# Optimization experiments

Measured on AMD Instinct MI355X. Metric: run time of the kernel, lower is better.

## Reference

```python
import jax, jax.numpy as jnp
import numpy as np

LN_EPS = 1e-5  # torch nn.LayerNorm default
ATT_EPS = 1e-8  # episilon added to sqrt(dk)

B, S, D = 16, 2048, 1024


def setup_inputs() -> dict:
    key = jax.random.key(0)
    ks = jax.random.split(key, 5)
    Q = jax.random.normal(ks[0], (B, S, D), dtype=jnp.float32)
    K = jax.random.normal(ks[1], (B, S, D), dtype=jnp.float32)
    V = jax.random.normal(ks[2], (B, S, D), dtype=jnp.float32)
    # xavier_normal for square DxD: std = sqrt(2/(D+D)) = 1/sqrt(D)
    std = 1.0 / np.sqrt(D)
    W1 = jax.random.normal(ks[3], (D, D), dtype=jnp.float32) * std
    W2 = jax.random.normal(ks[4], (D, D), dtype=jnp.float32) * std
    b1 = jnp.zeros((D,), dtype=jnp.float32)
    b2 = jnp.zeros((D,), dtype=jnp.float32)
    ln_gamma = jnp.ones((D,), dtype=jnp.float32)
    ln_beta = jnp.zeros((D,), dtype=jnp.float32)
    return {"Q": Q, "K": K, "V": V, "W1": W1, "b1": b1, "W2": W2, "b2": b2,
            "ln_gamma": ln_gamma, "ln_beta": ln_beta}


def _layer_norm(x, gamma, beta):
    mu = jnp.mean(x, axis=-1, keepdims=True)
    var = jnp.mean(jnp.square(x - mu), axis=-1, keepdims=True)
    return (x - mu) * jax.lax.rsqrt(var + LN_EPS) * gamma + beta


def reference(Q, K, V, W1, b1, W2, b2, ln_gamma, ln_beta):
    d = Q.shape[-1]
    scale = 1.0 / (jnp.sqrt(jnp.float32(max(1.0, d))) + ATT_EPS)
    # scores: (B, Sq, Sk)
    scores = jnp.einsum('bqd,bkd->bqk', Q, K) * scale
    attn = jax.nn.softmax(scores, axis=-1)
    V_att = jnp.einsum('bqk,bkd->bqd', attn, V)
    X = _layer_norm(Q + V_att, ln_gamma, ln_beta)
    ffn = jnp.einsum('bqd,ed->bqe', jax.nn.relu(jnp.einsum('bqd,hd->bqh', X, W1) + b1), W2) + b2
    return _layer_norm(ffn + X, ln_gamma, ln_beta)
```

## Files before the change

kernel.cpp:

```cpp
#include <hip/hip_runtime.h>
#include <cmath>
#include <cstdint>

#define LN_EPS 1e-5f

typedef __bf16 bf16x8 __attribute__((ext_vector_type(8)));
typedef float f32x4 __attribute__((ext_vector_type(4)));
typedef unsigned short u16x8 __attribute__((ext_vector_type(8)));
typedef unsigned short u16x4 __attribute__((ext_vector_type(4)));

__device__ inline float b2f(unsigned short u) {
    union { unsigned int ui; float f; } x; x.ui = ((unsigned int)u) << 16; return x.f;
}
__device__ inline unsigned short f2b(float f) {
    union { float f; unsigned int ui; } x; x.f = f;
    unsigned int u = x.ui;
    return (unsigned short)((u + 0x7FFFu + ((u >> 16) & 1u)) >> 16);
}

__global__ void cvt2_kernel(const float* __restrict__ ia, unsigned short* __restrict__ oa,
                            long na, float sa,
                            const float* __restrict__ ib, unsigned short* __restrict__ ob,
                            long nb) {
    long i = ((long)blockIdx.x * blockDim.x + threadIdx.x) * 8;
    long stride = (long)gridDim.x * blockDim.x * 8;
    long n = na + nb;
    for (; i < n; i += stride) {
        const float* in; unsigned short* out; long j; float s;
        if (i < na) { in = ia; out = oa; j = i; s = sa; }
        else        { in = ib; out = ob; j = i - na; s = 1.0f; }
        float4 a = *reinterpret_cast<const float4*>(in + j);
        float4 b = *reinterpret_cast<const float4*>(in + j + 4);
        u16x8 o;
        o[0] = f2b(a.x * s); o[1] = f2b(a.y * s); o[2] = f2b(a.z * s); o[3] = f2b(a.w * s);
        o[4] = f2b(b.x * s); o[5] = f2b(b.y * s); o[6] = f2b(b.z * s); o[7] = f2b(b.w * s);
        *reinterpret_cast<u16x8*>(out + j) = o;
    }
}

__global__ void transpose_kernel(const float* __restrict__ V, unsigned short* __restrict__ Vt,
                                 int S, int D) {
    __shared__ float t[32][33];
    int b = blockIdx.z;
    int s0 = blockIdx.x * 32, d0 = blockIdx.y * 32;
    int tx = threadIdx.x & 31, ty = threadIdx.x >> 5;
    const float* Vb = V + (long)b * S * D;
    unsigned short* Vtb = Vt + (long)b * S * D;
#pragma unroll
    for (int r = 0; r < 4; ++r)
        t[ty + r * 8][tx] = Vb[(long)(s0 + ty + r * 8) * D + d0 + tx];
    __syncthreads();
#pragma unroll
    for (int r = 0; r < 4; ++r)
        Vtb[(long)(d0 + ty + r * 8) * S + s0 + tx] = f2b(t[tx][ty + r * 8]);
}

#define GBK 64

__device__ inline void gload16(const unsigned short* g, unsigned short* l) {
    __builtin_amdgcn_global_load_lds((const __attribute__((address_space(1))) void*)g,
                                     (__attribute__((address_space(3))) void*)l, 16, 0, 0);
}

__device__ inline void stage_half(const unsigned short* gRowBase, int ldk, int k0,
                                  unsigned short* ldsHalf, int tid) {
#pragma unroll
    for (int l = 0; l < 2; ++l) {
        int g = l * 512 + tid;
        int row = g >> 3;
        int lg = (g & 7) ^ (row & 7);
        gload16(gRowBase + (long)row * ldk + k0 + lg * 8, ldsHalf + g * 8);
    }
}

__device__ inline bf16x8 frag_ld(const unsigned short* ldsHalf, int rowInHalf, int kgran) {
    int sw = kgran ^ (rowInHalf & 7);
    return *reinterpret_cast<const bf16x8*>(ldsHalf + rowInHalf * 64 + sw * 8);
}

#define GMFMA(am, bn, mi, ni) \
    acc[mi][ni] = __builtin_amdgcn_mfma_f32_16x16x32_bf16(am, bn, acc[mi][ni], 0, 0, 0)

template <int MODE>
__global__ __launch_bounds__(512, 1) void gemm256(
    const unsigned short* __restrict__ A, const unsigned short* __restrict__ B,
    void* __restrict__ Cout, const float* __restrict__ aux1, const float* __restrict__ aux2,
    float* __restrict__ aux3, float* __restrict__ aux4,
    int tX, int tY, int N, int K, long bsA, long bsB, long bsC, float scale) {
    extern __shared__ __align__(16) unsigned short lds[];
    const int cpx = gridDim.x >> 3;
    const int swz = (blockIdx.x & 7) * cpx + (blockIdx.x >> 3);
    const int bx = swz % tX;
    const int t2 = swz / tX;
    const int by = t2 % tY, bz = t2 / tY;

    const unsigned short* Ab = A + (long)bz * bsA + (long)by * 256 * K;
    const unsigned short* Bb = B + (long)bz * bsB + (long)bx * 256 * K;
    const int tid = threadIdx.x;
    const int wid = tid >> 6, lane = tid & 63;
    const int wr = wid >> 2, wc = wid & 3;
    const int lr = lane & 15, kq = lane >> 4;
    const int NT = K >> 6;
    const int ccol = lane & 15, crow0 = kq * 4;
    const long m0 = (long)by * 256 + wr * 128;
    const long n0 = (long)bx * 256 + wc * 64;
    const int bRow0 = (wc & 1) * 64;

#define STAGE_A(tile, half) stage_half(Ab + (long)(half) * 128 * K, K, (tile) * GBK, \
        lds + (((tile) & 1) * 32768 + (half) * 8192), tid)
#define STAGE_B(tile, half) stage_half(Bb + (long)(half) * 128 * K, K, (tile) * GBK, \
        lds + (((tile) & 1) * 32768 + 16384 + (half) * 8192), tid)

    f32x4 acc[8][4];
#pragma unroll
    for (int i = 0; i < 8; ++i)
#pragma unroll
        for (int j = 0; j < 4; ++j) acc[i][j] = (f32x4){0.f, 0.f, 0.f, 0.f};
    bf16x8 a[4][2], b[4][2];

    STAGE_A(0, 0); STAGE_A(0, 1); STAGE_B(0, 0); STAGE_B(0, 1);
    STAGE_B(1, 0); STAGE_A(1, 0);
    asm volatile("s_waitcnt vmcnt(4)" ::: "memory");
    __builtin_amdgcn_s_barrier();

    for (int t = 0; t < NT; ++t) {
        const unsigned short* aB = lds + ((t & 1) * 32768 + wr * 8192);
        const unsigned short* bB = lds + ((t & 1) * 32768 + 16384 + (wc >> 1) * 8192);
#pragma unroll
        for (int m = 0; m < 4; ++m)
#pragma unroll
            for (int ks = 0; ks < 2; ++ks)
                a[m][ks] = frag_ld(aB, m * 16 + lr, ks * 4 + kq);
#pragma unroll
        for (int n = 0; n < 2; ++n)
#pragma unroll
            for (int ks = 0; ks < 2; ++ks)
                b[n][ks] = frag_ld(bB, bRow0 + n * 16 + lr, ks * 4 + kq);
        if (t + 1 < NT) STAGE_A(t + 1, 1);
        __builtin_amdgcn_s_barrier();
        asm volatile("s_waitcnt lgkmcnt(0)" ::: "memory");
        __builtin_amdgcn_sched_barrier(0);
        __builtin_amdgcn_s_setprio(1);
#pragma unroll
        for (int m = 0; m < 4; ++m)
#pragma unroll
            for (int n = 0; n < 2; ++n)
#pragma unroll
                for (int ks = 0; ks < 2; ++ks) GMFMA(a[m][ks], b[n][ks], m, n);
        __builtin_amdgcn_s_setprio(0);
#pragma unroll
        for (int n = 0; n < 2; ++n)
#pragma unroll
            for (int ks = 0; ks < 2; ++ks)
                b[2 + n][ks] = frag_ld(bB, bRow0 + (2 + n) * 16 + lr, ks * 4 + kq);
        if (t + 1 < NT) STAGE_B(t + 1, 1);
        __builtin_amdgcn_s_barrier();
        asm volatile("s_waitcnt lgkmcnt(0)" ::: "memory");
        __builtin_amdgcn_sched_barrier(0);
        __builtin_amdgcn_s_setprio(1);
#pragma unroll
        for (int m = 0; m < 4; ++m)
#pragma unroll
            for (int n = 0; n < 2; ++n)
#pragma unroll
                for (int ks = 0; ks < 2; ++ks) GMFMA(a[m][ks], b[2 + n][ks], m, 2 + n);
        __builtin_amdgcn_s_setprio(0);
#pragma unroll
        for (int m = 0; m < 4; ++m)
#pragma unroll
            for (int ks = 0; ks < 2; ++ks)
                a[m][ks] = frag_ld(aB, 64 + m * 16 + lr, ks * 4 + kq);
        if (t + 2 < NT) { STAGE_B(t + 2, 0); STAGE_A(t + 2, 0); }
        if (t < NT - 2) asm volatile("s_waitcnt vmcnt(4)" ::: "memory");
        else            asm volatile("s_waitcnt vmcnt(0)" ::: "memory");
        __builtin_amdgcn_s_barrier();
        asm volatile("s_waitcnt lgkmcnt(0)" ::: "memory");
        __builtin_amdgcn_sched_barrier(0);
        __builtin_amdgcn_s_setprio(1);
#pragma unroll
        for (int m = 0; m < 4; ++m)
#pragma unroll
            for (int n = 0; n < 2; ++n)
#pragma unroll
                for (int ks = 0; ks < 2; ++ks) GMFMA(a[m][ks], b[n][ks], 4 + m, n);
#pragma unroll
        for (int m = 0; m < 4; ++m)
#pragma unroll
            for (int n = 0; n < 2; ++n)
#pragma unroll
                for (int ks = 0; ks < 2; ++ks) GMFMA(a[m][ks], b[2 + n][ks], 4 + m, 2 + n);
        __builtin_amdgcn_s_setprio(0);
    }

    if (MODE == 0) {
        float* sl = (float*)lds;
        unsigned short* Pout = (unsigned short*)Cout;
#pragma unroll
        for (int m = 0; m < 8; ++m) {
            float ls[4] = {0.f, 0.f, 0.f, 0.f};
#pragma unroll
            for (int n = 0; n < 4; ++n) {
                long gn = n0 + n * 16 + ccol;
#pragma unroll
                for (int r = 0; r < 4; ++r) {
                    float p = __expf(acc[m][n][r]);
                    ls[r] += p;
                    Pout[bz * bsC + (m0 + m * 16 + crow0 + r) * N + gn] = f2b(p);
                }
            }
#pragma unroll
            for (int r = 0; r < 4; ++r)
#pragma unroll
                for (int off = 8; off >= 1; off >>= 1) ls[r] += __shfl_xor(ls[r], off, 64);
            if ((lane & 15) == 0)
#pragma unroll
                for (int r = 0; r < 4; ++r)
                    sl[wc * 256 + wr * 128 + m * 16 + crow0 + r] = ls[r];
        }
        __syncthreads();
        if (wc == 0) {
#pragma unroll
            for (int rep = 0; rep < 2; ++rep) {
                int rowB = wr * 128 + rep * 64 + lane;
                float s4 = sl[0 * 256 + rowB] + sl[1 * 256 + rowB] +
                           sl[2 * 256 + rowB] + sl[3 * 256 + rowB];
                ((float*)aux1)[((long)bz * 8 + bx) * 2048 + by * 256 + rowB] = s4;
            }
        }
        return;
    }

    if (MODE == 1) {
        const float* il = aux2 + (long)bz * 2048 + m0;
        float* sls = (float*)lds;
        float* slq = sls + 1024;
        unsigned short* Xout = (unsigned short*)Cout;
#pragma unroll
        for (int m = 0; m < 8; ++m) {
            float ls[4] = {0.f, 0.f, 0.f, 0.f}, lq[4] = {0.f, 0.f, 0.f, 0.f};
#pragma unroll
            for (int r = 0; r < 4; ++r) {
                float cf = il[m * 16 + crow0 + r];
                long gm = m0 + m * 16 + crow0 + r;
#pragma unroll
                for (int n = 0; n < 4; ++n) {
                    long gn = n0 + n * 16 + ccol;
                    long idx = bz * bsC + gm * N + gn;
                    float v = acc[m][n][r] * cf +
                              b2f(((const unsigned short*)aux1)[idx]) * scale;
                    Xout[idx] = f2b(v);
                    ls[r] += v; lq[r] += v * v;
                }
            }
#pragma unroll
            for (int r = 0; r < 4; ++r)
#pragma unroll
                for (int off = 8; off >= 1; off >>= 1) {
                    ls[r] += __shfl_xor(ls[r], off, 64);
                    lq[r] += __shfl_xor(lq[r], off, 64);
                }
            if ((lane & 15) == 0)
#pragma unroll
                for (int r = 0; r < 4; ++r) {
                    sls[wc * 256 + wr * 128 + m * 16 + crow0 + r] = ls[r];
                    slq[wc * 256 + wr * 128 + m * 16 + crow0 + r] = lq[r];
                }
        }
        __syncthreads();
        if (wc == 0) {
#pragma unroll
            for (int rep = 0; rep < 2; ++rep) {
                int rowB = wr * 128 + rep * 64 + lane;
                float s4 = sls[rowB] + sls[256 + rowB] + sls[512 + rowB] + sls[768 + rowB];
                float q4 = slq[rowB] + slq[256 + rowB] + slq[512 + rowB] + slq[768 + rowB];
                long sidx = ((long)bz * 4 + bx) * 2048 + by * 256 + rowB;
                aux3[sidx] = s4;
                aux4[sidx] = q4;
            }
        }
        return;
    }

#pragma unroll
    for (int m = 0; m < 8; ++m) {
#pragma unroll
        for (int n = 0; n < 4; ++n) {
            long gn = n0 + n * 16 + ccol;
#pragma unroll
            for (int r = 0; r < 4; ++r) {
                long gm = m0 + m * 16 + crow0 + r;
                float v = acc[m][n][r];
                if (MODE == 2) {
                    ((unsigned short*)Cout)[gm * N + gn] = f2b(fmaxf(v + aux1[gn], 0.f));
                } else {
                    long idx = gm * N + gn;
                    ((unsigned short*)Cout)[idx] =
                        f2b(v + aux1[gn] + b2f(((const unsigned short*)aux2)[idx]));
                }
            }
        }
    }
#undef STAGE_A
#undef STAGE_B
}

__global__ void suminv_kernel(const float* __restrict__ stats, float* __restrict__ invL) {
    int i = blockIdx.x * 256 + threadIdx.x;
    int bz = i >> 11, row = i & 2047;
    long base = (long)bz * 8 * 2048 + row;
    float L = 0.f;
#pragma unroll
    for (int t = 0; t < 8; ++t) L += stats[base + t * 2048];
    invL[i] = 1.f / L;
}

__global__ void ln_apply_kernel(unsigned short* __restrict__ X, const float* __restrict__ ss,
                                const float* __restrict__ sq, const float* __restrict__ gamma,
                                const float* __restrict__ beta) {
    __shared__ float mr[4];
    int tid = threadIdx.x;
    long rowbase = (long)blockIdx.x * 2;
    if (tid < 2) {
        long row = rowbase + tid;
        int bz = (int)(row >> 11), lrow = (int)(row & 2047);
        long base = (long)bz * 4 * 2048 + lrow;
        float s = 0.f, q = 0.f;
#pragma unroll
        for (int t = 0; t < 4; ++t) { s += ss[base + t * 2048]; q += sq[base + t * 2048]; }
        float m = s * (1.f / 1024.f);
        float var = q * (1.f / 1024.f) - m * m;
        mr[tid * 2] = m;
        mr[tid * 2 + 1] = rsqrtf(var + LN_EPS);
    }
    __syncthreads();
    int sub = tid >> 7;
    float m = mr[sub * 2], r = mr[sub * 2 + 1];
    long i = rowbase * 1024 + (long)tid * 8;
    int col = (tid * 8) & 1023;
    u16x8 raw = *reinterpret_cast<const u16x8*>(X + i);
    float4 g0 = *reinterpret_cast<const float4*>(gamma + col);
    float4 g1 = *reinterpret_cast<const float4*>(gamma + col + 4);
    float4 b0 = *reinterpret_cast<const float4*>(beta + col);
    float4 b1 = *reinterpret_cast<const float4*>(beta + col + 4);
    u16x8 o;
    o[0] = f2b((b2f(raw[0]) - m) * r * g0.x + b0.x);
    o[1] = f2b((b2f(raw[1]) - m) * r * g0.y + b0.y);
    o[2] = f2b((b2f(raw[2]) - m) * r * g0.z + b0.z);
    o[3] = f2b((b2f(raw[3]) - m) * r * g0.w + b0.w);
    o[4] = f2b((b2f(raw[4]) - m) * r * g1.x + b1.x);
    o[5] = f2b((b2f(raw[5]) - m) * r * g1.y + b1.y);
    o[6] = f2b((b2f(raw[6]) - m) * r * g1.z + b1.z);
    o[7] = f2b((b2f(raw[7]) - m) * r * g1.w + b1.w);
    *reinterpret_cast<u16x8*>(X + i) = o;
}

__device__ inline float wave_sum(float v) {
#pragma unroll
    for (int off = 32; off > 0; off >>= 1) v += __shfl_xor(v, off, 64);
    return v;
}

__global__ void ln_final_kernel(const unsigned short* __restrict__ Yb,
                                const float* __restrict__ gamma, const float* __restrict__ beta,
                                float* __restrict__ out) {
    __shared__ float red[8];
    long row = blockIdx.x;
    const unsigned short* y = Yb + row * 1024;
    int tid = threadIdx.x;
    int wv = tid >> 6, ln = tid & 63;
    u16x4 raw = *reinterpret_cast<const u16x4*>(y + tid * 4);
    float v0 = b2f(raw[0]), v1 = b2f(raw[1]), v2 = b2f(raw[2]), v3 = b2f(raw[3]);
    float s = v0 + v1 + v2 + v3;
    float q = v0 * v0 + v1 * v1 + v2 * v2 + v3 * v3;
    s = wave_sum(s);
    q = wave_sum(q);
    if (ln == 0) { red[wv] = s; red[4 + wv] = q; }
    __syncthreads();
    s = red[0] + red[1] + red[2] + red[3];
    q = red[4] + red[5] + red[6] + red[7];
    float mu = s * (1.f / 1024.f);
    float var = q * (1.f / 1024.f) - mu * mu;
    float rsg = rsqrtf(var + LN_EPS);
    float4 g = *reinterpret_cast<const float4*>(gamma + tid * 4);
    float4 b = *reinterpret_cast<const float4*>(beta + tid * 4);
    float4 o;
    o.x = (v0 - mu) * rsg * g.x + b.x;
    o.y = (v1 - mu) * rsg * g.y + b.y;
    o.z = (v2 - mu) * rsg * g.z + b.z;
    o.w = (v3 - mu) * rsg * g.w + b.w;
    *reinterpret_cast<float4*>(out + row * 1024 + tid * 4) = o;
}

extern "C" void kernel_launch(void* const* d_in, const int* in_sizes, int n_in,
                              void* d_out, int out_size, void* d_ws, size_t ws_size,
                              hipStream_t stream) {
    const float* Q     = (const float*)d_in[0];
    const float* Kin   = (const float*)d_in[1];
    const float* V     = (const float*)d_in[2];
    const float* W1    = (const float*)d_in[3];
    const float* b1    = (const float*)d_in[4];
    const float* W2    = (const float*)d_in[5];
    const float* b2    = (const float*)d_in[6];
    const float* gamma = (const float*)d_in[7];
    const float* beta  = (const float*)d_in[8];
    float* out = (float*)d_out;

    const int Bq = 16, S = 2048, D = 1024;
    const long SD = (long)S * D;
    const long SS = (long)S * S;
    const long rows = (long)Bq * S;

    const size_t NEED = 3 * (size_t)(Bq * SD * 2) + 2 * (size_t)D * D * 2 + (size_t)(Bq * SS * 2);
    if (ws_size < NEED) return;

    char* ws = (char*)d_ws;
    unsigned short* Qb  = (unsigned short*)ws; ws += Bq * SD * 2;
    unsigned short* Kb  = (unsigned short*)ws; ws += Bq * SD * 2;
    unsigned short* Vt  = (unsigned short*)ws; ws += Bq * SD * 2;
    unsigned short* W1b = (unsigned short*)ws; ws += (long)D * D * 2;
    unsigned short* W2b = (unsigned short*)ws; ws += (long)D * D * 2;
    unsigned short* Sb  = (unsigned short*)ws; ws += Bq * SS * 2;

    unsigned short* Xb = Qb;
    unsigned short* H  = Kb;
    unsigned short* Yb = (unsigned short*)Sb;

    char* sc = (char*)W1b;
    float* stats   = (float*)sc;
    float* invL    = (float*)(sc + 0x100000);
    float* stats_s = (float*)(sc + 0x140000);
    float* stats_q = (float*)(sc + 0x1C0000);

    const int DYN_LDS = 131072;
    (void)hipFuncSetAttribute(reinterpret_cast<const void*>(&gemm256<0>),
                              hipFuncAttributeMaxDynamicSharedMemorySize, DYN_LDS);
    (void)hipFuncSetAttribute(reinterpret_cast<const void*>(&gemm256<1>),
                              hipFuncAttributeMaxDynamicSharedMemorySize, DYN_LDS);
    (void)hipFuncSetAttribute(reinterpret_cast<const void*>(&gemm256<2>),
                              hipFuncAttributeMaxDynamicSharedMemorySize, DYN_LDS);
    (void)hipFuncSetAttribute(reinterpret_cast<const void*>(&gemm256<3>),
                              hipFuncAttributeMaxDynamicSharedMemorySize, DYN_LDS);

    const float scale = 1.0f / (sqrtf((float)D) + 1e-8f);
    const float rescale = sqrtf((float)D) + 1e-8f;

    cvt2_kernel<<<2048, 256, 0, stream>>>(Q, Qb, Bq * SD, scale, Kin, Kb, Bq * SD);
    transpose_kernel<<<dim3(S / 32, D / 32, Bq), 256, 0, stream>>>(V, Vt, S, D);

    gemm256<0><<<1024, 512, DYN_LDS, stream>>>(
        Qb, Kb, Sb, stats, nullptr, nullptr, nullptr, 8, 8, S, D, SD, SD, SS, 1.0f);
    suminv_kernel<<<128, 256, 0, stream>>>(stats, invL);

    gemm256<1><<<512, 512, DYN_LDS, stream>>>(
        Sb, Vt, Xb, (const float*)Qb, invL, stats_s, stats_q, 4, 8, D, S, SS, SD, SD, rescale);
    ln_apply_kernel<<<16384, 256, 0, stream>>>(Xb, stats_s, stats_q, gamma, beta);

    cvt2_kernel<<<512, 256, 0, stream>>>(W1, W1b, (long)D * D, 1.0f, W2, W2b, (long)D * D);

    gemm256<2><<<512, 512, DYN_LDS, stream>>>(
        Xb, W1b, H, b1, nullptr, nullptr, nullptr, 4, 128, D, D, 0, 0, 0, 1.0f);
    gemm256<3><<<512, 512, DYN_LDS, stream>>>(
        H, W2b, Yb, b2, (const float*)Xb, nullptr, nullptr, 4, 128, D, D, 0, 0, 0, 1.0f);
    ln_final_kernel<<<rows, 256, 0, stream>>>(Yb, gamma, beta, out);
}
```

Measured before the change: 631.0 us.

## Software-pipeline LDS fragment loads one phase ahead of MFMA in GEMM loop

Restructures the GEMM main loop so that register fragments for the next phase (and the first phase of the next tile) are loaded from LDS while the current MFMA batch runs. It does this with separate alo/ahi/b01/b23 register sets and by dropping the explicit lgkmcnt(0) waits and sched_barriers. Global staging issues are spread across four phases instead of three. The goal is to hide LDS read latency behind matrix-core work. The cost is extra VGPR pressure and reliance on compiler-inserted waits, which may hurt occupancy or ordering.

```diff
diff --git a/kernel.cpp b/kernel.cpp
--- a/kernel.cpp
+++ b/kernel.cpp
@@ -116,81 +116,97 @@
     for (int i = 0; i < 8; ++i)
 #pragma unroll
         for (int j = 0; j < 4; ++j) acc[i][j] = (f32x4){0.f, 0.f, 0.f, 0.f};
-    bf16x8 a[4][2], b[4][2];
+    bf16x8 alo[4][2], ahi[4][2], b01[2][2], b23[2][2];
 
     STAGE_A(0, 0); STAGE_A(0, 1); STAGE_B(0, 0); STAGE_B(0, 1);
     STAGE_B(1, 0); STAGE_A(1, 0);
     asm volatile("s_waitcnt vmcnt(4)" ::: "memory");
     __builtin_amdgcn_s_barrier();
 
+    {
+        const unsigned short* aB = lds + wr * 8192;
+        const unsigned short* bB = lds + 16384 + (wc >> 1) * 8192;
+#pragma unroll
+        for (int m = 0; m < 4; ++m)
+#pragma unroll
+            for (int ks = 0; ks < 2; ++ks) alo[m][ks] = frag_ld(aB, m * 16 + lr, ks * 4 + kq);
+#pragma unroll
+        for (int n = 0; n < 2; ++n)
+#pragma unroll
+            for (int ks = 0; ks < 2; ++ks) b01[n][ks] = frag_ld(bB, bRow0 + n * 16 + lr, ks * 4 + kq);
+    }
+
     for (int t = 0; t < NT; ++t) {
         const unsigned short* aB = lds + ((t & 1) * 32768 + wr * 8192);
         const unsigned short* bB = lds + ((t & 1) * 32768 + 16384 + (wc >> 1) * 8192);
 #pragma unroll
-        for (int m = 0; m < 4; ++m)
+        for (int n = 0; n < 2; ++n)
 #pragma unroll
             for (int ks = 0; ks < 2; ++ks)
-                a[m][ks] = frag_ld(aB, m * 16 + lr, ks * 4 + kq);
-#pragma unroll
-        for (int n = 0; n < 2; ++n)
+                b23[n][ks] = frag_ld(bB, bRow0 + (2 + n) * 16 + lr, ks * 4 + kq);
+        if (t + 1 < NT) STAGE_A(t + 1, 1);
+        __builtin_amdgcn_s_setprio(1);
+#pragma unroll
+        for (int m = 0; m < 4; ++m)
+#pragma unroll
+            for (int n = 0; n < 2; ++n)
+#pragma unroll
+                for (int ks = 0; ks < 2; ++ks) GMFMA(alo[m][ks], b01[n][ks], m, n);
+        __builtin_amdgcn_s_setprio(0);
+        __builtin_amdgcn_s_barrier();
+#pragma unroll
+        for (int m = 0; m < 4; ++m)
 #pragma unroll
             for (int ks = 0; ks < 2; ++ks)
-                b[n][ks] = frag_ld(bB, bRow0 + n * 16 + lr, ks * 4 + kq);
-        if (t + 1 < NT) STAGE_A(t + 1, 1);
+                ahi[m][ks] = frag_ld(aB, 64 + m * 16 + lr, ks * 4 + kq);
+        if (t + 1 < NT) STAGE_B(t + 1, 1);
+        __builtin_amdgcn_s_setprio(1);
+#pragma unroll
+        for (int m = 0; m < 4; ++m)
+#pragma unroll
+            for (int n = 0; n < 2; ++n)
+#pragma unroll
+                for (int ks = 0; ks < 2; ++ks) GMFMA(alo[m][ks], b23[n][ks], m, 2 + n);
+        __builtin_amdgcn_s_setprio(0);
         __builtin_amdgcn_s_barrier();
-        asm volatile("s_waitcnt lgkmcnt(0)" ::: "memory");
-        __builtin_amdgcn_sched_barrier(0);
+        if (t + 2 < NT) STAGE_B(t + 2, 0);
         __builtin_amdgcn_s_setprio(1);
 #pragma unroll
         for (int m = 0; m < 4; ++m)
 #pragma unroll
             for (int n = 0; n < 2; ++n)
 #pragma unroll
-                for (int ks = 0; ks < 2; ++ks) GMFMA(a[m][ks], b[n][ks], m, n);
+                for (int ks = 0; ks < 2; ++ks) GMFMA(ahi[m][ks], b01[n][ks], 4 + m, n);
         __builtin_amdgcn_s_setprio(0);
-#pragma unroll
-        for (int n = 0; n < 2; ++n)
-#pragma unroll
-            for (int ks = 0; ks < 2; ++ks)
-                b[2 + n][ks] = frag_ld(bB, bRow0 + (2 + n) * 16 + lr, ks * 4 + kq);
-        if (t + 1 < NT) STAGE_B(t + 1, 1);
         __builtin_amdgcn_s_barrier();
-        asm volatile("s_waitcnt lgkmcnt(0)" ::: "memory");
-        __builtin_amdgcn_sched_barrier(0);
-        __builtin_amdgcn_s_setprio(1);
-#pragma unroll
-        for (int m = 0; m < 4; ++m)
-#pragma unroll
-            for (int n = 0; n < 2; ++n)
-#pragma unroll
-                for (int ks = 0; ks < 2; ++ks) GMFMA(a[m][ks], b[2 + n][ks], m, 2 + n);
-        __builtin_amdgcn_s_setprio(0);
-#pragma unroll
-        for (int m = 0; m < 4; ++m)
-#pragma unroll
-            for (int ks = 0; ks < 2; ++ks)
-                a[m][ks] = frag_ld(aB, 64 + m * 16 + lr, ks * 4 + kq);
-        if (t + 2 < NT) { STAGE_B(t + 2, 0); STAGE_A(t + 2, 0); }
+        if (t + 2 < NT) STAGE_A(t + 2, 0);
         if (t < NT - 2) asm volatile("s_waitcnt vmcnt(4)" ::: "memory");
         else            asm volatile("s_waitcnt vmcnt(0)" ::: "memory");
         __builtin_amdgcn_s_barrier();
-        asm volatile("s_waitcnt lgkmcnt(0)" ::: "memory");
-        __builtin_amdgcn_sched_barrier(0);
+        if (t + 1 < NT) {
+            const unsigned short* aBn = lds + (((t + 1) & 1) * 32768 + wr * 8192);
+            const unsigned short* bBn = lds + (((t + 1) & 1) * 32768 + 16384 + (wc >> 1) * 8192);
+#pragma unroll
+            for (int m = 0; m < 4; ++m)
+#pragma unroll
+                for (int ks = 0; ks < 2; ++ks)
+                    alo[m][ks] = frag_ld(aBn, m * 16 + lr, ks * 4 + kq);
+#pragma unroll
+            for (int n = 0; n < 2; ++n)
+#pragma unroll
+                for (int ks = 0; ks < 2; ++ks)
+                    b01[n][ks] = frag_ld(bBn, bRow0 + n * 16 + lr, ks * 4 + kq);
+        }
         __builtin_amdgcn_s_setprio(1);
 #pragma unroll
         for (int m = 0; m < 4; ++m)
 #pragma unroll
             for (int n = 0; n < 2; ++n)
 #pragma unroll
-                for (int ks = 0; ks < 2; ++ks) GMFMA(a[m][ks], b[n][ks], 4 + m, n);
-#pragma unroll
-        for (int m = 0; m < 4; ++m)
-#pragma unroll
-            for (int n = 0; n < 2; ++n)
-#pragma unroll
-                for (int ks = 0; ks < 2; ++ks) GMFMA(a[m][ks], b[2 + n][ks], 4 + m, 2 + n);
+                for (int ks = 0; ks < 2; ++ks) GMFMA(ahi[m][ks], b23[n][ks], 4 + m, 2 + n);
         __builtin_amdgcn_s_setprio(0);
     }
+    __builtin_amdgcn_s_barrier();
 
     if (MODE == 0) {
         float* sl = (float*)lds;
```

After: 618.4 us, median of 3. -2.0%, faster.
